# Kernel optimization log

Hardware: AMD Instinct MI355X
Metric: run time of the kernel (lower is better)

The kernel has to match this reference:

```python
import jax, jax.numpy as jnp
import numpy as np

SCALE = 8.0  # sqrt(d_k), d_k = 64
NEG_INF = -1000000000.0


def setup_inputs() -> dict:
    key = jax.random.key(0)
    ks = jax.random.split(key, 7)
    B, H, S, D = 2, 8, 4096, 64
    shp = (B, H, S, D)
    q_a = jax.random.normal(ks[0], shp, dtype=jnp.float32)
    k_a = jax.random.normal(ks[1], shp, dtype=jnp.float32)
    v_a = jax.random.normal(ks[2], shp, dtype=jnp.float32)
    q_s = jax.random.normal(ks[3], shp, dtype=jnp.float32)
    k_s = jax.random.normal(ks[4], shp, dtype=jnp.float32)
    v_s = jax.random.normal(ks[5], shp, dtype=jnp.float32)
    mask = jax.random.randint(ks[6], (B, 1, 1, S), 0, 2, dtype=jnp.int32)
    return {"q_a": q_a, "k_a": k_a, "v_a": v_a,
            "q_s": q_s, "k_s": k_s, "v_s": v_s, "mask": mask}


def reference(q_a, k_a, v_a, q_s, k_s, v_s, mask):
    # a2a + a2s + s2a + s2s == (q_a + q_s) @ (k_a + k_s)^T  (exact algebra)
    q = q_a + q_s                               # [B,H,S,D]
    k = k_a + k_s                               # [B,H,S,D]
    score = jnp.einsum("bhqd,bhkd->bhqk", q, k) / SCALE  # [B,H,S,S]
    score = jnp.where(mask == 0, NEG_INF, score)
    attn = jax.nn.softmax(score, axis=-1)       # dropout p=0 (eval/identity)
    out = jnp.einsum("bhqk,bhkd->bhqd", attn, v_a + v_s)
    return out
```

## Files before the change

### kernel.cpp

```cpp
#include <hip/hip_runtime.h>
#include <hip/hip_bf16.h>

#define S_   4096
#define D_   64
#define BH_  16
#define QW   64
#define QBLK 256
#define KVB  128
#define NCH  2

typedef __attribute__((ext_vector_type(8)))  short short8_t;
typedef __attribute__((ext_vector_type(16))) float f32x16;
#define QSCALE 0.18033688011112042f

__device__ __forceinline__ unsigned short f2bf(float f) {
  unsigned u = __float_as_uint(f);
  u += 0x7fffu + ((u >> 16) & 1u);
  return (unsigned short)(u >> 16);
}

__device__ __forceinline__ void glds16(const unsigned short* g, unsigned short* l) {
  __builtin_amdgcn_global_load_lds(
      (const __attribute__((address_space(1))) unsigned int*)g,
      (__attribute__((address_space(3))) unsigned int*)l, 16, 0, 0);
}

__global__ void kvgather_kernel(const float* __restrict__ ka, const float* __restrict__ ks,
                                const float* __restrict__ va, const float* __restrict__ vs,
                                const float* __restrict__ qa, const float* __restrict__ qs,
                                const int* __restrict__ mask, int* __restrict__ cnt,
                                unsigned short* __restrict__ qhat,
                                unsigned short* __restrict__ khat,
                                unsigned short* __restrict__ vt) {
  __shared__ int ps[256];
  __shared__ int srcLds[64];
  __shared__ __align__(16) unsigned short t[D_][72];
  const int bh = blockIdx.y, b = bh >> 3;
  const int s0 = blockIdx.x * 64;
  const int tid = threadIdx.x;

  const int* mb = mask + (size_t)b * S_;
  int m[16], c = 0;
  const int base = tid * 16;
#pragma unroll
  for (int i = 0; i < 16; ++i) { m[i] = mb[base + i]; c += (m[i] != 0); }
  ps[tid] = c;
  __syncthreads();
  for (int off = 1; off < 256; off <<= 1) {
    int add = (tid >= off) ? ps[tid - off] : 0;
    __syncthreads();
    ps[tid] += add;
    __syncthreads();
  }
  const int C = ps[255];
  int pos = ps[tid] - c;
#pragma unroll
  for (int i = 0; i < 16; ++i) {
    if (m[i]) {
      int r = pos++;
      if (r >= s0 && r < s0 + 64) srcLds[r - s0] = base + i;
    }
  }
  if (tid == 0 && blockIdx.x == 0 && (bh & 7) == 0) cnt[b] = C;
  __syncthreads();

  const int row16 = tid >> 4;
  const int col4  = (tid & 15) * 4;
#pragma unroll
  for (int p = 0; p < 4; ++p) {
    int srow = p * 16 + row16;
    int j = s0 + srow;
    {
      size_t qoff = ((size_t)bh * S_ + j) * D_ + col4;
      float4 xq = *(const float4*)(qa + qoff);
      float4 yq = *(const float4*)(qs + qoff);
      ushort4 rq;
      rq.x = f2bf((xq.x + yq.x) * QSCALE); rq.y = f2bf((xq.y + yq.y) * QSCALE);
      rq.z = f2bf((xq.z + yq.z) * QSCALE); rq.w = f2bf((xq.w + yq.w) * QSCALE);
      *(ushort4*)(qhat + qoff) = rq;
    }
    float4 xv = {0, 0, 0, 0}, yv = {0, 0, 0, 0};
    float4 xk = {0, 0, 0, 0}, yk = {0, 0, 0, 0};
    if (j < C) {
      int src = srcLds[srow];
      size_t off = ((size_t)bh * S_ + src) * D_ + col4;
      xv = *(const float4*)(va + off);
      yv = *(const float4*)(vs + off);
      xk = *(const float4*)(ka + off);
      yk = *(const float4*)(ks + off);
    }
    t[col4 + 0][srow] = f2bf(xv.x + yv.x);
    t[col4 + 1][srow] = f2bf(xv.y + yv.y);
    t[col4 + 2][srow] = f2bf(xv.z + yv.z);
    t[col4 + 3][srow] = f2bf(xv.w + yv.w);
    ushort4 rk;
    rk.x = f2bf(xk.x + yk.x); rk.y = f2bf(xk.y + yk.y);
    rk.z = f2bf(xk.z + yk.z); rk.w = f2bf(xk.w + yk.w);
    *(ushort4*)(khat + ((size_t)bh * S_ + j) * D_ + col4) = rk;
  }
  __syncthreads();
#pragma unroll
  for (int r = 0; r < 2; ++r) {
    int e = (r * 256 + tid) * 8;
    int d = e >> 6, sc = e & 63;
    short8_t v = *(const short8_t*)&t[d][sc];
    *(short8_t*)(vt + ((size_t)bh * D_ + d) * S_ + s0 + sc) = v;
  }
}

__global__ __launch_bounds__(512, 1) void attn_kernel(
    const unsigned short* __restrict__ Qb, const unsigned short* __restrict__ Kb,
    const unsigned short* __restrict__ Vt, const int* __restrict__ cnt,
    float* __restrict__ out) {
  __shared__ __align__(16) unsigned char smem[131072];
  unsigned short* lKp = (unsigned short*)smem;
  unsigned short* lVp = lKp + 32768;

  const int tid  = threadIdx.x;
  const int wave = tid >> 6;
  const int chid = wave >> 2;
  const int wq   = wave & 3;
  const int ctid = tid & 255;
  const int lane = tid & 63;
  const int l31  = lane & 31;
  const int h5   = lane >> 5;
  const int rsw  = l31 & 7;
  const int bh   = blockIdx.y;
  const int qrow0 = blockIdx.x * QBLK + wq * QW + l31;
  const int b    = bh >> 3;
  const int C    = cnt[b];
  const int NTt  = (C + KVB - 1) / KVB;
  const int tpc  = (NTt + NCH - 1) / NCH;
  const int ts   = chid * tpc;
  const int te   = (ts + tpc < NTt) ? (ts + tpc) : NTt;

  short8_t qf[2][4];
#pragma unroll
  for (int qb = 0; qb < 2; ++qb) {
    const unsigned short* qp = Qb + ((size_t)bh * S_ + qrow0 + 32 * qb) * D_ + h5 * 8;
#pragma unroll
    for (int t4 = 0; t4 < 4; ++t4) qf[qb][t4] = *(const short8_t*)(qp + t4 * 16);
  }

  short8_t ones8;
#pragma unroll
  for (int i = 0; i < 8; ++i) ones8[i] = (short)0x3F80;

  const unsigned short* gk0 = Kb + (size_t)bh * S_ * D_;
  const unsigned short* gv0 = Vt + (size_t)bh * D_ * S_;

  int srcK[4], srcV[4], ldsB[4];
#pragma unroll
  for (int r2 = 0; r2 < 4; ++r2) {
    int c = r2 * 256 + ctid;
    int rowK = c >> 3, gK = (c & 7) ^ (rowK & 7);
    srcK[r2] = rowK * 64 + gK * 8;
    int rowV = c >> 4, gg = c & 15;
    int swg = (gg & 8) | ((gg & 7) ^ (rowV & 7));
    srcV[r2] = rowV * S_ + swg * 8;
    ldsB[r2] = r2 * 2048 + wq * 512;
  }
  unsigned short* lK0 = lKp + chid * 2 * 8192;
  unsigned short* lV0 = lVp + chid * 2 * 8192;

  f32x16 acc0[2], acc1[2], accS[2];
  float mrow[2];
#pragma unroll
  for (int qb = 0; qb < 2; ++qb) {
    acc0[qb] = (f32x16)(0.0f); acc1[qb] = (f32x16)(0.0f); accS[qb] = (f32x16)(0.0f);
    mrow[qb] = -1e30f;
  }

  if (ts < te) {
#pragma unroll
    for (int r2 = 0; r2 < 4; ++r2) {
      glds16(gk0 + (size_t)ts * KVB * D_ + srcK[r2], lK0 + ldsB[r2]);
      glds16(gv0 + ts * KVB + srcV[r2], lV0 + ldsB[r2]);
    }
  }

  for (int it = 0; it < tpc; ++it) {
    const int t = ts + it;
    const int cur = it & 1;
    if (t + 1 < te) {
#pragma unroll
      for (int r2 = 0; r2 < 4; ++r2) {
        glds16(gk0 + (size_t)(t + 1) * KVB * D_ + srcK[r2], lK0 + (cur ^ 1) * 8192 + ldsB[r2]);
        glds16(gv0 + (t + 1) * KVB + srcV[r2], lV0 + (cur ^ 1) * 8192 + ldsB[r2]);
      }
      asm volatile("s_waitcnt vmcnt(8)" ::: "memory");
    } else {
      asm volatile("s_waitcnt vmcnt(0)" ::: "memory");
    }
    __builtin_amdgcn_s_barrier();
    __builtin_amdgcn_sched_barrier(0);

    if (t < te) {
      const unsigned short* lK = lK0 + cur * 8192;
      const unsigned short* lV = lV0 + cur * 8192;
#pragma unroll
      for (int h = 0; h < 2; ++h) {
        f32x16 sv0[2], sv1[2];
#pragma unroll
        for (int qb = 0; qb < 2; ++qb) { sv0[qb] = (f32x16)(0.0f); sv1[qb] = (f32x16)(0.0f); }
        __builtin_amdgcn_s_setprio(1);
#pragma unroll
        for (int t4 = 0; t4 < 4; ++t4) {
          int g = ((2 * t4 + h5) ^ rsw) * 8;
          short8_t kf0 = *(const short8_t*)&lK[(h * 64 + l31) * 64 + g];
          short8_t kf1 = *(const short8_t*)&lK[(h * 64 + 32 + l31) * 64 + g];
          sv0[0] = __builtin_amdgcn_mfma_f32_32x32x16_bf16(kf0, qf[0][t4], sv0[0], 0, 0, 0);
          sv0[1] = __builtin_amdgcn_mfma_f32_32x32x16_bf16(kf0, qf[1][t4], sv0[1], 0, 0, 0);
          sv1[0] = __builtin_amdgcn_mfma_f32_32x32x16_bf16(kf1, qf[0][t4], sv1[0], 0, 0, 0);
          sv1[1] = __builtin_amdgcn_mfma_f32_32x32x16_bf16(kf1, qf[1][t4], sv1[1], 0, 0, 0);
        }
        __builtin_amdgcn_s_setprio(0);

        if (t == NTt - 1) {
          int kvb = t * KVB + h * 64;
#pragma unroll
          for (int i = 0; i < 16; ++i) {
            int key = kvb + (i & 3) + 8 * (i >> 2) + 4 * h5;
#pragma unroll
            for (int qb = 0; qb < 2; ++qb) {
              if (key >= C) sv0[qb][i] = -1e9f;
              if (key + 32 >= C) sv1[qb][i] = -1e9f;
            }
          }
        }

        unsigned int pkw[2][16];
#pragma unroll
        for (int qb = 0; qb < 2; ++qb) {
          float tmx[8];
#pragma unroll
          for (int i = 0; i < 8; ++i)
            tmx[i] = fmaxf(fmaxf(sv0[qb][i], sv0[qb][i + 8]),
                           fmaxf(sv1[qb][i], sv1[qb][i + 8]));
#pragma unroll
          for (int i = 0; i < 4; ++i) tmx[i] = fmaxf(tmx[i], tmx[i + 4]);
          float tm = fmaxf(fmaxf(tmx[0], tmx[1]), fmaxf(tmx[2], tmx[3]));
          tm = fmaxf(tm, __shfl_xor(tm, 32));

          if (__any(tm > mrow[qb] + 8.0f)) {
            float mnew = fmaxf(mrow[qb], tm);
            float sc = __builtin_amdgcn_exp2f(mrow[qb] - mnew);
            mrow[qb] = mnew;
            accS[qb][0] *= sc;
#pragma unroll
            for (int i = 0; i < 16; ++i) { acc0[qb][i] *= sc; acc1[qb][i] *= sc; }
          }

          float m = mrow[qb];
#pragma unroll
          for (int i = 0; i < 16; i += 4) {
            sv0[qb][i + 0] = __builtin_amdgcn_exp2f(sv0[qb][i + 0] - m);
            sv0[qb][i + 1] = __builtin_amdgcn_exp2f(sv0[qb][i + 1] - m);
            sv0[qb][i + 2] = __builtin_amdgcn_exp2f(sv0[qb][i + 2] - m);
            sv0[qb][i + 3] = __builtin_amdgcn_exp2f(sv0[qb][i + 3] - m);
            sv1[qb][i + 0] = __builtin_amdgcn_exp2f(sv1[qb][i + 0] - m);
            sv1[qb][i + 1] = __builtin_amdgcn_exp2f(sv1[qb][i + 1] - m);
            sv1[qb][i + 2] = __builtin_amdgcn_exp2f(sv1[qb][i + 2] - m);
            sv1[qb][i + 3] = __builtin_amdgcn_exp2f(sv1[qb][i + 3] - m);
          }

#pragma unroll
          for (int rg = 0; rg < 4; ++rg) {
            __hip_bfloat162 a0 = __float22bfloat162_rn({sv0[qb][rg * 4 + 0], sv0[qb][rg * 4 + 1]});
            __hip_bfloat162 a1 = __float22bfloat162_rn({sv0[qb][rg * 4 + 2], sv0[qb][rg * 4 + 3]});
            __hip_bfloat162 b0 = __float22bfloat162_rn({sv1[qb][rg * 4 + 0], sv1[qb][rg * 4 + 1]});
            __hip_bfloat162 b1 = __float22bfloat162_rn({sv1[qb][rg * 4 + 2], sv1[qb][rg * 4 + 3]});
            pkw[qb][rg * 2 + 0] = *(unsigned int*)&a0;
            pkw[qb][rg * 2 + 1] = *(unsigned int*)&a1;
            pkw[qb][8 + rg * 2 + 0] = *(unsigned int*)&b0;
            pkw[qb][8 + rg * 2 + 1] = *(unsigned int*)&b1;
          }
        }

        __builtin_amdgcn_s_setprio(1);
#pragma unroll
        for (int kt = 0; kt < 4; ++kt) {
          const int n = kt >> 1, k1 = kt & 1;
          int gcol = ((h * 8) | ((2 * kt + h5) ^ rsw)) * 8;
          short8_t vf0 = *(const short8_t*)&lV[l31 * KVB + gcol];
          short8_t vf1 = *(const short8_t*)&lV[(32 + l31) * KVB + gcol];
#pragma unroll
          for (int qb = 0; qb < 2; ++qb) {
            unsigned int sA = pkw[qb][n * 8 + (2 * k1 + h5) * 2 + 0];
            unsigned int sB = pkw[qb][n * 8 + (2 * k1 + h5) * 2 + 1];
            unsigned int xA = pkw[qb][n * 8 + (2 * k1 + (h5 ^ 1)) * 2 + 0];
            unsigned int xB = pkw[qb][n * 8 + (2 * k1 + (h5 ^ 1)) * 2 + 1];
            unsigned int pA = (unsigned int)__shfl_xor((int)xA, 32);
            unsigned int pB = (unsigned int)__shfl_xor((int)xB, 32);
            union { unsigned int u[4]; short8_t v; } bb;
            bb.u[0] = h5 ? pA : sA;
            bb.u[1] = h5 ? pB : sB;
            bb.u[2] = h5 ? sA : pA;
            bb.u[3] = h5 ? sB : pB;
            acc0[qb] = __builtin_amdgcn_mfma_f32_32x32x16_bf16(vf0, bb.v, acc0[qb], 0, 0, 0);
            acc1[qb] = __builtin_amdgcn_mfma_f32_32x32x16_bf16(vf1, bb.v, acc1[qb], 0, 0, 0);
            accS[qb] = __builtin_amdgcn_mfma_f32_32x32x16_bf16(ones8, bb.v, accS[qb], 0, 0, 0);
          }
        }
        __builtin_amdgcn_s_setprio(0);
      }
    }

    __builtin_amdgcn_sched_barrier(0);
    __builtin_amdgcn_s_barrier();
  }

  float* part = (float*)smem;
  float2* mlsh = (float2*)(smem + 73728);
  __syncthreads();

  if (chid == 1) {
#pragma unroll
    for (int qb = 0; qb < 2; ++qb) {
      int rl = wq * 64 + qb * 32 + l31;
      float* pr = part + rl * 72;
#pragma unroll
      for (int rg = 0; rg < 4; ++rg) {
        float4 o0, o1;
        o0.x = acc0[qb][rg * 4 + 0]; o0.y = acc0[qb][rg * 4 + 1];
        o0.z = acc0[qb][rg * 4 + 2]; o0.w = acc0[qb][rg * 4 + 3];
        o1.x = acc1[qb][rg * 4 + 0]; o1.y = acc1[qb][rg * 4 + 1];
        o1.z = acc1[qb][rg * 4 + 2]; o1.w = acc1[qb][rg * 4 + 3];
        *(float4*)(pr + rg * 8 + h5 * 4) = o0;
        *(float4*)(pr + 32 + rg * 8 + h5 * 4) = o1;
      }
      if (h5 == 0) { float2 st; st.x = mrow[qb]; st.y = accS[qb][0]; mlsh[rl] = st; }
    }
  }
  __syncthreads();
  if (chid == 0) {
#pragma unroll
    for (int qb = 0; qb < 2; ++qb) {
      int rl = wq * 64 + qb * 32 + l31;
      float2 pml = mlsh[rl];
      float m0 = mrow[qb], l0 = accS[qb][0];
      float M = fmaxf(m0, pml.x);
      float w0 = exp2f(m0 - M), w1 = exp2f(pml.x - M);
      float inv = 1.0f / (l0 * w0 + pml.y * w1);
      w0 *= inv; w1 *= inv;
      const float* pr = part + rl * 72;
      float* op = out + ((size_t)bh * S_ + qrow0 + 32 * qb) * D_;
#pragma unroll
      for (int rg = 0; rg < 4; ++rg) {
        float4 p0v = *(const float4*)(pr + rg * 8 + h5 * 4);
        float4 p1v = *(const float4*)(pr + 32 + rg * 8 + h5 * 4);
        float4 o0, o1;
        o0.x = acc0[qb][rg * 4 + 0] * w0 + p0v.x * w1;
        o0.y = acc0[qb][rg * 4 + 1] * w0 + p0v.y * w1;
        o0.z = acc0[qb][rg * 4 + 2] * w0 + p0v.z * w1;
        o0.w = acc0[qb][rg * 4 + 3] * w0 + p0v.w * w1;
        o1.x = acc1[qb][rg * 4 + 0] * w0 + p1v.x * w1;
        o1.y = acc1[qb][rg * 4 + 1] * w0 + p1v.y * w1;
        o1.z = acc1[qb][rg * 4 + 2] * w0 + p1v.z * w1;
        o1.w = acc1[qb][rg * 4 + 3] * w0 + p1v.w * w1;
        *(float4*)(op + rg * 8 + h5 * 4) = o0;
        *(float4*)(op + 32 + rg * 8 + h5 * 4) = o1;
      }
    }
  }
}

extern "C" void kernel_launch(void* const* d_in, const int* in_sizes, int n_in,
                              void* d_out, int out_size, void* d_ws, size_t ws_size,
                              hipStream_t stream) {
  const float* q_a = (const float*)d_in[0];
  const float* k_a = (const float*)d_in[1];
  const float* v_a = (const float*)d_in[2];
  const float* q_s = (const float*)d_in[3];
  const float* k_s = (const float*)d_in[4];
  const float* v_s = (const float*)d_in[5];
  const int*   mask = (const int*)d_in[6];
  float* out = (float*)d_out;
  (void)in_sizes; (void)n_in; (void)out_size; (void)ws_size;

  const int N = BH_ * S_ * D_;
  unsigned short* qhat = (unsigned short*)d_ws;
  unsigned short* khat = qhat + N;
  unsigned short* vt   = khat + N;
  int* cnt = (int*)(vt + N);

  {
    dim3 g(S_ / 64, BH_);
    kvgather_kernel<<<g, 256, 0, stream>>>(k_a, k_s, v_a, v_s, q_a, q_s, mask, cnt,
                                           qhat, khat, vt);
  }
  {
    dim3 g(S_ / QBLK, BH_);
    attn_kernel<<<g, 512, 0, stream>>>(qhat, khat, vt, cnt, out);
  }
}
```

Before: 109.3 us.

## Software-pipeline QK of second half-tile ahead of PV of first half

Restructures the per-tile inner loop so the QK^T MFMAs for the second 64-key half are issued before the PV MFMAs of the first half. The softmax and pack work and the PV step move into inline helpers. The aim is to interleave independent matrix work with softmax VALU work and so shorten dependency stalls. In exchange, score accumulators for both halves are live at once, which raises register pressure and risks spills.

```diff
diff --git a/kernel.cpp b/kernel.cpp
--- a/kernel.cpp
+++ b/kernel.cpp
@@ -106,6 +106,96 @@
     short8_t v = *(const short8_t*)&t[d][sc];
     *(short8_t*)(vt + ((size_t)bh * D_ + d) * S_ + s0 + sc) = v;
   }
+}
+
+__device__ __forceinline__ void smpack(
+    f32x16 (&s0)[2], f32x16 (&s1)[2],
+    f32x16 (&a0)[2], f32x16 (&a1)[2], f32x16 (&aS)[2], float (&mr)[2],
+    unsigned int (&pk)[2][16], bool dopad, int kvb, int C, int h5) {
+#pragma unroll
+  for (int qb = 0; qb < 2; ++qb) {
+    if (dopad) {
+#pragma unroll
+      for (int i = 0; i < 16; ++i) {
+        int key = kvb + (i & 3) + 8 * (i >> 2) + 4 * h5;
+        if (key >= C) s0[qb][i] = -1e9f;
+        if (key + 32 >= C) s1[qb][i] = -1e9f;
+      }
+    }
+    float tmx[8];
+#pragma unroll
+    for (int i = 0; i < 8; ++i)
+      tmx[i] = fmaxf(fmaxf(s0[qb][i], s0[qb][i + 8]), fmaxf(s1[qb][i], s1[qb][i + 8]));
+#pragma unroll
+    for (int i = 0; i < 4; ++i) tmx[i] = fmaxf(tmx[i], tmx[i + 4]);
+    float tm = fmaxf(fmaxf(tmx[0], tmx[1]), fmaxf(tmx[2], tmx[3]));
+    tm = fmaxf(tm, __shfl_xor(tm, 32));
+
+    if (__any(tm > mr[qb] + 8.0f)) {
+      float mnew = fmaxf(mr[qb], tm);
+      float sc = __builtin_amdgcn_exp2f(mr[qb] - mnew);
+      mr[qb] = mnew;
+      aS[qb][0] *= sc;
+#pragma unroll
+      for (int i = 0; i < 16; ++i) { a0[qb][i] *= sc; a1[qb][i] *= sc; }
+    }
+
+    float m = mr[qb];
+#pragma unroll
+    for (int i = 0; i < 16; i += 4) {
+      s0[qb][i + 0] = __builtin_amdgcn_exp2f(s0[qb][i + 0] - m);
+      s0[qb][i + 1] = __builtin_amdgcn_exp2f(s0[qb][i + 1] - m);
+      s0[qb][i + 2] = __builtin_amdgcn_exp2f(s0[qb][i + 2] - m);
+      s0[qb][i + 3] = __builtin_amdgcn_exp2f(s0[qb][i + 3] - m);
+      s1[qb][i + 0] = __builtin_amdgcn_exp2f(s1[qb][i + 0] - m);
+      s1[qb][i + 1] = __builtin_amdgcn_exp2f(s1[qb][i + 1] - m);
+      s1[qb][i + 2] = __builtin_amdgcn_exp2f(s1[qb][i + 2] - m);
+      s1[qb][i + 3] = __builtin_amdgcn_exp2f(s1[qb][i + 3] - m);
+    }
+#pragma unroll
+    for (int rg = 0; rg < 4; ++rg) {
+      __hip_bfloat162 a0p = __float22bfloat162_rn({s0[qb][rg * 4 + 0], s0[qb][rg * 4 + 1]});
+      __hip_bfloat162 a1p = __float22bfloat162_rn({s0[qb][rg * 4 + 2], s0[qb][rg * 4 + 3]});
+      __hip_bfloat162 b0p = __float22bfloat162_rn({s1[qb][rg * 4 + 0], s1[qb][rg * 4 + 1]});
+      __hip_bfloat162 b1p = __float22bfloat162_rn({s1[qb][rg * 4 + 2], s1[qb][rg * 4 + 3]});
+      pk[qb][rg * 2 + 0] = *(unsigned int*)&a0p;
+      pk[qb][rg * 2 + 1] = *(unsigned int*)&a1p;
+      pk[qb][8 + rg * 2 + 0] = *(unsigned int*)&b0p;
+      pk[qb][8 + rg * 2 + 1] = *(unsigned int*)&b1p;
+    }
+  }
+}
+
+__device__ __forceinline__ void pvstep(
+    const unsigned short* lV, int h, unsigned int (&pk)[2][16],
+    f32x16 (&a0)[2], f32x16 (&a1)[2], f32x16 (&aS)[2],
+    short8_t ones8, int l31, int h5, int rsw) {
+  __builtin_amdgcn_s_setprio(1);
+#pragma unroll
+  for (int kt = 0; kt < 4; ++kt) {
+    const int n = kt >> 1, k1 = kt & 1;
+    int gcol = ((h * 8) | ((2 * kt + h5) ^ rsw)) * 8;
+    short8_t vf0 = *(const short8_t*)&lV[l31 * KVB + gcol];
+    short8_t vf1 = *(const short8_t*)&lV[(32 + l31) * KVB + gcol];
+#pragma unroll
+    for (int qb = 0; qb < 2; ++qb) {
+      unsigned int sA = pk[qb][n * 8 + (2 * k1 + h5) * 2 + 0];
+      unsigned int sB = pk[qb][n * 8 + (2 * k1 + h5) * 2 + 1];
+      unsigned int xA = pk[qb][n * 8 + (2 * k1 + (h5 ^ 1)) * 2 + 0];
+      unsigned int xB = pk[qb][n * 8 + (2 * k1 + (h5 ^ 1)) * 2 + 1];
+      unsigned int pA = (unsigned int)__shfl_xor((int)xA, 32);
+      unsigned int pB = (unsigned int)__shfl_xor((int)xB, 32);
+      union { unsigned int u[4]; short8_t v; } bb;
+      bb.u[0] = h5 ? pA : sA;
+      bb.u[1] = h5 ? pB : sB;
+      bb.u[2] = h5 ? sA : pA;
+      bb.u[3] = h5 ? sB : pB;
+      a0[qb] = __builtin_amdgcn_mfma_f32_32x32x16_bf16(vf0, bb.v, a0[qb], 0, 0, 0);
+      a1[qb] = __builtin_amdgcn_mfma_f32_32x32x16_bf16(vf1, bb.v, a1[qb], 0, 0, 0);
+      aS[qb] = __builtin_amdgcn_mfma_f32_32x32x16_bf16(ones8, bb.v, aS[qb], 0, 0, 0);
+    }
+  }
+  __builtin_amdgcn_s_setprio(0);
 }
 
 __global__ __launch_bounds__(512, 1) void attn_kernel(
@@ -198,112 +288,48 @@
     if (t < te) {
       const unsigned short* lK = lK0 + cur * 8192;
       const unsigned short* lV = lV0 + cur * 8192;
-#pragma unroll
-      for (int h = 0; h < 2; ++h) {
-        f32x16 sv0[2], sv1[2];
-#pragma unroll
-        for (int qb = 0; qb < 2; ++qb) { sv0[qb] = (f32x16)(0.0f); sv1[qb] = (f32x16)(0.0f); }
-        __builtin_amdgcn_s_setprio(1);
-#pragma unroll
-        for (int t4 = 0; t4 < 4; ++t4) {
-          int g = ((2 * t4 + h5) ^ rsw) * 8;
-          short8_t kf0 = *(const short8_t*)&lK[(h * 64 + l31) * 64 + g];
-          short8_t kf1 = *(const short8_t*)&lK[(h * 64 + 32 + l31) * 64 + g];
-          sv0[0] = __builtin_amdgcn_mfma_f32_32x32x16_bf16(kf0, qf[0][t4], sv0[0], 0, 0, 0);
-          sv0[1] = __builtin_amdgcn_mfma_f32_32x32x16_bf16(kf0, qf[1][t4], sv0[1], 0, 0, 0);
-          sv1[0] = __builtin_amdgcn_mfma_f32_32x32x16_bf16(kf1, qf[0][t4], sv1[0], 0, 0, 0);
-          sv1[1] = __builtin_amdgcn_mfma_f32_32x32x16_bf16(kf1, qf[1][t4], sv1[1], 0, 0, 0);
-        }
-        __builtin_amdgcn_s_setprio(0);
-
-        if (t == NTt - 1) {
-          int kvb = t * KVB + h * 64;
-#pragma unroll
-          for (int i = 0; i < 16; ++i) {
-            int key = kvb + (i & 3) + 8 * (i >> 2) + 4 * h5;
-#pragma unroll
-            for (int qb = 0; qb < 2; ++qb) {
-              if (key >= C) sv0[qb][i] = -1e9f;
-              if (key + 32 >= C) sv1[qb][i] = -1e9f;
-            }
-          }
-        }
-
-        unsigned int pkw[2][16];
-#pragma unroll
-        for (int qb = 0; qb < 2; ++qb) {
-          float tmx[8];
-#pragma unroll
-          for (int i = 0; i < 8; ++i)
-            tmx[i] = fmaxf(fmaxf(sv0[qb][i], sv0[qb][i + 8]),
-                           fmaxf(sv1[qb][i], sv1[qb][i + 8]));
-#pragma unroll
-          for (int i = 0; i < 4; ++i) tmx[i] = fmaxf(tmx[i], tmx[i + 4]);
-          float tm = fmaxf(fmaxf(tmx[0], tmx[1]), fmaxf(tmx[2], tmx[3]));
-          tm = fmaxf(tm, __shfl_xor(tm, 32));
-
-          if (__any(tm > mrow[qb] + 8.0f)) {
-            float mnew = fmaxf(mrow[qb], tm);
-            float sc = __builtin_amdgcn_exp2f(mrow[qb] - mnew);
-            mrow[qb] = mnew;
-            accS[qb][0] *= sc;
-#pragma unroll
-            for (int i = 0; i < 16; ++i) { acc0[qb][i] *= sc; acc1[qb][i] *= sc; }
-          }
-
-          float m = mrow[qb];
-#pragma unroll
-          for (int i = 0; i < 16; i += 4) {
-            sv0[qb][i + 0] = __builtin_amdgcn_exp2f(sv0[qb][i + 0] - m);
-            sv0[qb][i + 1] = __builtin_amdgcn_exp2f(sv0[qb][i + 1] - m);
-            sv0[qb][i + 2] = __builtin_amdgcn_exp2f(sv0[qb][i + 2] - m);
-            sv0[qb][i + 3] = __builtin_amdgcn_exp2f(sv0[qb][i + 3] - m);
-            sv1[qb][i + 0] = __builtin_amdgcn_exp2f(sv1[qb][i + 0] - m);
-            sv1[qb][i + 1] = __builtin_amdgcn_exp2f(sv1[qb][i + 1] - m);
-            sv1[qb][i + 2] = __builtin_amdgcn_exp2f(sv1[qb][i + 2] - m);
-            sv1[qb][i + 3] = __builtin_amdgcn_exp2f(sv1[qb][i + 3] - m);
-          }
-
-#pragma unroll
-          for (int rg = 0; rg < 4; ++rg) {
-            __hip_bfloat162 a0 = __float22bfloat162_rn({sv0[qb][rg * 4 + 0], sv0[qb][rg * 4 + 1]});
-            __hip_bfloat162 a1 = __float22bfloat162_rn({sv0[qb][rg * 4 + 2], sv0[qb][rg * 4 + 3]});
-            __hip_bfloat162 b0 = __float22bfloat162_rn({sv1[qb][rg * 4 + 0], sv1[qb][rg * 4 + 1]});
-            __hip_bfloat162 b1 = __float22bfloat162_rn({sv1[qb][rg * 4 + 2], sv1[qb][rg * 4 + 3]});
-            pkw[qb][rg * 2 + 0] = *(unsigned int*)&a0;
-            pkw[qb][rg * 2 + 1] = *(unsigned int*)&a1;
-            pkw[qb][8 + rg * 2 + 0] = *(unsigned int*)&b0;
-            pkw[qb][8 + rg * 2 + 1] = *(unsigned int*)&b1;
-          }
-        }
-
-        __builtin_amdgcn_s_setprio(1);
-#pragma unroll
-        for (int kt = 0; kt < 4; ++kt) {
-          const int n = kt >> 1, k1 = kt & 1;
-          int gcol = ((h * 8) | ((2 * kt + h5) ^ rsw)) * 8;
-          short8_t vf0 = *(const short8_t*)&lV[l31 * KVB + gcol];
-          short8_t vf1 = *(const short8_t*)&lV[(32 + l31) * KVB + gcol];
-#pragma unroll
-          for (int qb = 0; qb < 2; ++qb) {
-            unsigned int sA = pkw[qb][n * 8 + (2 * k1 + h5) * 2 + 0];
-            unsigned int sB = pkw[qb][n * 8 + (2 * k1 + h5) * 2 + 1];
-            unsigned int xA = pkw[qb][n * 8 + (2 * k1 + (h5 ^ 1)) * 2 + 0];
-            unsigned int xB = pkw[qb][n * 8 + (2 * k1 + (h5 ^ 1)) * 2 + 1];
-            unsigned int pA = (unsigned int)__shfl_xor((int)xA, 32);
-            unsigned int pB = (unsigned int)__shfl_xor((int)xB, 32);
-            union { unsigned int u[4]; short8_t v; } bb;
-            bb.u[0] = h5 ? pA : sA;
-            bb.u[1] = h5 ? pB : sB;
-            bb.u[2] = h5 ? sA : pA;
-            bb.u[3] = h5 ? sB : pB;
-            acc0[qb] = __builtin_amdgcn_mfma_f32_32x32x16_bf16(vf0, bb.v, acc0[qb], 0, 0, 0);
-            acc1[qb] = __builtin_amdgcn_mfma_f32_32x32x16_bf16(vf1, bb.v, acc1[qb], 0, 0, 0);
-            accS[qb] = __builtin_amdgcn_mfma_f32_32x32x16_bf16(ones8, bb.v, accS[qb], 0, 0, 0);
-          }
-        }
-        __builtin_amdgcn_s_setprio(0);
-      }
+      const bool tail = (t == NTt - 1);
+      unsigned int pkw[2][16];
+
+      f32x16 sv0[2], sv1[2];
+#pragma unroll
+      for (int qb = 0; qb < 2; ++qb) { sv0[qb] = (f32x16)(0.0f); sv1[qb] = (f32x16)(0.0f); }
+      __builtin_amdgcn_s_setprio(1);
+#pragma unroll
+      for (int t4 = 0; t4 < 4; ++t4) {
+        int g = ((2 * t4 + h5) ^ rsw) * 8;
+        short8_t kf0 = *(const short8_t*)&lK[l31 * 64 + g];
+        short8_t kf1 = *(const short8_t*)&lK[(32 + l31) * 64 + g];
+        sv0[0] = __builtin_amdgcn_mfma_f32_32x32x16_bf16(kf0, qf[0][t4], sv0[0], 0, 0, 0);
+        sv0[1] = __builtin_amdgcn_mfma_f32_32x32x16_bf16(kf0, qf[1][t4], sv0[1], 0, 0, 0);
+        sv1[0] = __builtin_amdgcn_mfma_f32_32x32x16_bf16(kf1, qf[0][t4], sv1[0], 0, 0, 0);
+        sv1[1] = __builtin_amdgcn_mfma_f32_32x32x16_bf16(kf1, qf[1][t4], sv1[1], 0, 0, 0);
+      }
+      __builtin_amdgcn_s_setprio(0);
+
+      smpack(sv0, sv1, acc0, acc1, accS, mrow, pkw, tail, t * KVB, C, h5);
+
+      f32x16 tv0[2], tv1[2];
+#pragma unroll
+      for (int qb = 0; qb < 2; ++qb) { tv0[qb] = (f32x16)(0.0f); tv1[qb] = (f32x16)(0.0f); }
+      __builtin_amdgcn_s_setprio(1);
+#pragma unroll
+      for (int t4 = 0; t4 < 4; ++t4) {
+        int g = ((2 * t4 + h5) ^ rsw) * 8;
+        short8_t kf0 = *(const short8_t*)&lK[(64 + l31) * 64 + g];
+        short8_t kf1 = *(const short8_t*)&lK[(64 + 32 + l31) * 64 + g];
+        tv0[0] = __builtin_amdgcn_mfma_f32_32x32x16_bf16(kf0, qf[0][t4], tv0[0], 0, 0, 0);
+        tv0[1] = __builtin_amdgcn_mfma_f32_32x32x16_bf16(kf0, qf[1][t4], tv0[1], 0, 0, 0);
+        tv1[0] = __builtin_amdgcn_mfma_f32_32x32x16_bf16(kf1, qf[0][t4], tv1[0], 0, 0, 0);
+        tv1[1] = __builtin_amdgcn_mfma_f32_32x32x16_bf16(kf1, qf[1][t4], tv1[1], 0, 0, 0);
+      }
+      __builtin_amdgcn_s_setprio(0);
+
+      pvstep(lV, 0, pkw, acc0, acc1, accS, ones8, l31, h5, rsw);
+
+      smpack(tv0, tv1, acc0, acc1, accS, mrow, pkw, tail, t * KVB + 64, C, h5);
+
+      pvstep(lV, 1, pkw, acc0, acc1, accS, ones8, l31, h5, rsw);
     }
 
     __builtin_amdgcn_sched_barrier(0);
```

Result: slower. 155.5 us (+42.3%).
